# Performance work log

Hardware: AMD Instinct MI355X
Metric: run time of the kernel (lower is better)

Reference implementation:

```python
import jax, jax.numpy as jnp
import numpy as np

IN_FEATURES = 4096
OUT_FEATURES = 4096
BLOCK_SIZE = 16
E2M1_VALUES = jnp.array([0.0, 0.5, 1.0, 1.5, 2.0, 3.0, 4.0, 6.0], dtype=jnp.float32)


def dequantize_nvfp4(weight_packed, weight_scales, out_features, in_features, block_size, dtype):
    # Unpack two 4-bit codes per byte: even positions = high nibble, odd = low nibble
    p = weight_packed.astype(jnp.int32)
    high = (p >> 4) & 15
    low = p & 15
    unpacked = jnp.stack([high, low], axis=-1).reshape(-1)  # [out*in]
    sign = ((unpacked >> 3) & 1).astype(dtype)
    mag_code = unpacked & 7
    magnitude = E2M1_VALUES.astype(dtype)[mag_code]
    vals = jnp.where(sign == 1, -magnitude, magnitude)
    # Expand per-block E4M3 scales (repeat_interleave)
    scales_expanded = jnp.repeat(weight_scales.astype(dtype), block_size)
    w = vals * scales_expanded
    return w.reshape(out_features, in_features)


def setup_inputs() -> dict:
    key = jax.random.key(0)
    k1, k2, k3, k4 = jax.random.split(key, 4)
    x = jax.random.normal(k1, (4, 2048, IN_FEATURES), dtype=jnp.float32)
    weight_packed = jax.random.randint(k2, (OUT_FEATURES * IN_FEATURES // 2,), 0, 256, dtype=jnp.int32)
    weight_scales = jax.random.uniform(k3, (OUT_FEATURES * IN_FEATURES // BLOCK_SIZE,), dtype=jnp.float32)
    bias = jax.random.normal(k4, (OUT_FEATURES,), dtype=jnp.float32)
    return {"x": x, "weight_packed": weight_packed, "weight_scales": weight_scales, "bias": bias}


def reference(x, weight_packed, weight_scales, bias):
    w = dequantize_nvfp4(weight_packed, weight_scales, OUT_FEATURES, IN_FEATURES, BLOCK_SIZE, x.dtype)
    # F.linear: y = x @ w.T + bias
    return jnp.einsum('bsi,oi->bso', x, w) + bias
```

## Files before the change

kernel.cpp:

```cpp
#include <hip/hip_runtime.h>
#include <cstdint>
#include <cstddef>

#define MDIM 8192
#define NDIM 4096
#define KDIM 4096

typedef __attribute__((ext_vector_type(8))) __bf16 bf16x8;
typedef __attribute__((ext_vector_type(4))) float floatx4;

typedef __attribute__((address_space(3))) void lds_t;
typedef __attribute__((address_space(1))) void glb_t;

__device__ __forceinline__ unsigned short f32_to_bf16(float f) {
  unsigned int u = __float_as_uint(f);
  u += 0x7FFFu + ((u >> 16) & 1u);
  return (unsigned short)(u >> 16);
}

__device__ __forceinline__ float fp4_mag(int c) {
  int e = (c >> 1) & 3, m = c & 1;
  int sh = e ? (e - 1) : 0;
  return e ? 0.5f * (float)((2 + m) << sh) : 0.5f * (float)m;
}

__global__ __launch_bounds__(256) void conv_x_kernel(const float* __restrict__ x,
                                                     unsigned short* __restrict__ xb) {
  const int t = blockIdx.x * 256 + threadIdx.x;
  const float4* src = (const float4*)x + (size_t)t * 2;
  float4 a = src[0], b = src[1];
  union { unsigned short us[8]; uint4 u4; } o;
  o.us[0] = f32_to_bf16(a.x); o.us[1] = f32_to_bf16(a.y);
  o.us[2] = f32_to_bf16(a.z); o.us[3] = f32_to_bf16(a.w);
  o.us[4] = f32_to_bf16(b.x); o.us[5] = f32_to_bf16(b.y);
  o.us[6] = f32_to_bf16(b.z); o.us[7] = f32_to_bf16(b.w);
  ((uint4*)xb)[t] = o.u4;
}

__global__ __launch_bounds__(256) void dequant_kernel(const int* __restrict__ packed,
                                                      const float* __restrict__ scales,
                                                      unsigned short* __restrict__ wb) {
  const int t = blockIdx.x * 256 + threadIdx.x;
  const int4* p = (const int4*)packed + (size_t)t * 2;
  int4 pa = p[0], pb = p[1];
  float s = scales[t];
  int bytes[8] = {pa.x, pa.y, pa.z, pa.w, pb.x, pb.y, pb.z, pb.w};
  union { unsigned short us[16]; uint4 u4[2]; } o;
#pragma unroll
  for (int i = 0; i < 8; ++i) {
    int by = bytes[i] & 255;
    int hi = by >> 4, lo = by & 15;
    float vh = fp4_mag(hi & 7) * s; if (hi & 8) vh = -vh;
    float vl = fp4_mag(lo & 7) * s; if (lo & 8) vl = -vl;
    o.us[2 * i]     = f32_to_bf16(vh);
    o.us[2 * i + 1] = f32_to_bf16(vl);
  }
  uint4* dst = (uint4*)(wb + (size_t)t * 16);
  dst[0] = o.u4[0]; dst[1] = o.u4[1];
}

__global__ __launch_bounds__(512) void gemm256_kernel(const __bf16* __restrict__ A,
                                                      const __bf16* __restrict__ B,
                                                      const float* __restrict__ bias,
                                                      float* __restrict__ C) {
  __shared__ __bf16 ldsbuf[65536];
  __bf16* As = ldsbuf;
  __bf16* Bs = ldsbuf + 32768;

  const int t = threadIdx.x;
  const int wave = t >> 6, lane = t & 63;
  const int quad = lane >> 4, r16 = lane & 15;
  const int wr = wave >> 2, wc = wave & 3;

  const int bid = blockIdx.x;
  const int wg = (bid & 7) * 64 + (bid >> 3);
  const int m0 = (wg >> 4) * 256, n0 = (wg & 15) * 256;

  const int swzS = ((t >> 3) & 7) << 4;
  const int b0 = (t * 16) ^ swzS;
  const int b1 = (8192 + t * 16) ^ swzS;
  const int row0 = b0 >> 6, col0 = (b0 & 63) >> 1;
  const int row1 = b1 >> 6, col1 = (b1 & 63) >> 1;

  const __bf16* pa0 = A + (size_t)(m0 + row0) * KDIM + col0;
  const __bf16* pa1 = A + (size_t)(m0 + row1) * KDIM + col1;
  const __bf16* pb0 = B + (size_t)(n0 + row0) * KDIM + col0;
  const __bf16* pb1 = B + (size_t)(n0 + row1) * KDIM + col1;

  const int swzR = ((r16 >> 1) & 7) << 4;
  const int offAe = ((((wr * 128 + r16) * 64) + quad * 16) ^ swzR) >> 1;
  const int offBe = ((((wc * 64  + r16) * 64) + quad * 16) ^ swzR) >> 1;

  floatx4 acc[8][4] = {};

#define STAGE(TT) do {                                                                              \
    const int _kk = (TT) * 32;                                                                      \
    __bf16* _ab = As + ((TT) & 3) * 8192;                                                           \
    __bf16* _bb = Bs + ((TT) & 3) * 8192;                                                           \
    __builtin_amdgcn_global_load_lds((const glb_t*)(pa0 + _kk), (lds_t*)(_ab + wave * 512), 16, 0, 0);        \
    __builtin_amdgcn_global_load_lds((const glb_t*)(pa1 + _kk), (lds_t*)(_ab + 4096 + wave * 512), 16, 0, 0); \
    __builtin_amdgcn_global_load_lds((const glb_t*)(pb0 + _kk), (lds_t*)(_bb + wave * 512), 16, 0, 0);        \
    __builtin_amdgcn_global_load_lds((const glb_t*)(pb1 + _kk), (lds_t*)(_bb + 4096 + wave * 512), 16, 0, 0); \
  } while (0)

#define BARRIER() asm volatile("s_barrier" ::: "memory")

#define COMPUTE(TT) do {                                                          \
    const __bf16* _a = As + ((TT) & 3) * 8192;                                    \
    const __bf16* _b = Bs + ((TT) & 3) * 8192;                                    \
    bf16x8 af[8], bfv[4];                                                         \
    _Pragma("unroll")                                                             \
    for (int i = 0; i < 8; ++i) af[i] = *(const bf16x8*)(_a + offAe + i * 512);   \
    _Pragma("unroll")                                                             \
    for (int j = 0; j < 4; ++j) bfv[j] = *(const bf16x8*)(_b + offBe + j * 512);  \
    __builtin_amdgcn_s_setprio(1);                                                \
    _Pragma("unroll")                                                             \
    for (int i = 0; i < 8; ++i) {                                                 \
      _Pragma("unroll")                                                           \
      for (int j = 0; j < 4; ++j)                                                 \
        acc[i][j] = __builtin_amdgcn_mfma_f32_16x16x32_bf16(af[i], bfv[j], acc[i][j], 0, 0, 0); \
    }                                                                             \
    __builtin_amdgcn_s_setprio(0);                                                \
    BARRIER();                                                                    \
  } while (0)

  STAGE(0); STAGE(1); STAGE(2);

  for (int T = 0; T < 125; ++T) {
    STAGE(T + 3);
    asm volatile("s_waitcnt vmcnt(12)" ::: "memory");
    BARRIER();
    COMPUTE(T);
  }
  asm volatile("s_waitcnt vmcnt(8)" ::: "memory");
  BARRIER();
  COMPUTE(125);
  asm volatile("s_waitcnt vmcnt(4)" ::: "memory");
  BARRIER();
  COMPUTE(126);
  asm volatile("s_waitcnt vmcnt(0)" ::: "memory");
  BARRIER();
  COMPUTE(127);

#undef STAGE
#undef BARRIER
#undef COMPUTE

  float bv[4];
#pragma unroll
  for (int j = 0; j < 4; ++j) bv[j] = bias[n0 + wc * 64 + j * 16 + r16];
#pragma unroll
  for (int i = 0; i < 8; ++i) {
    const int gm = m0 + wr * 128 + i * 16 + quad * 4;
#pragma unroll
    for (int j = 0; j < 4; ++j) {
      float* cp = C + (size_t)gm * NDIM + (n0 + wc * 64 + j * 16 + r16);
#pragma unroll
      for (int r = 0; r < 4; ++r)
        cp[(size_t)r * NDIM] = acc[i][j][r] + bv[j];
    }
  }
}

__global__ __launch_bounds__(256) void fused_fallback(const float* __restrict__ x,
                                                      const int* __restrict__ packed,
                                                      const float* __restrict__ scales,
                                                      const float* __restrict__ bias,
                                                      float* __restrict__ out) {
  const int n = blockIdx.x * 256 + threadIdx.x;
  const int m = blockIdx.y;
  const float* xr = x + (size_t)m * KDIM;
  const int* pr = packed + (size_t)n * (KDIM / 2);
  const float* sc = scales + (size_t)n * (KDIM / 16);
  float acc = 0.f;
  for (int kb = 0; kb < KDIM / 16; ++kb) {
    float s = sc[kb];
    float part = 0.f;
#pragma unroll
    for (int i = 0; i < 8; ++i) {
      int by = pr[kb * 8 + i] & 255;
      int hi = by >> 4, lo = by & 15;
      float vh = fp4_mag(hi & 7); if (hi & 8) vh = -vh;
      float vl = fp4_mag(lo & 7); if (lo & 8) vl = -vl;
      part += xr[kb * 16 + 2 * i] * vh + xr[kb * 16 + 2 * i + 1] * vl;
    }
    acc += s * part;
  }
  out[(size_t)m * NDIM + n] = acc + bias[n];
}

extern "C" void kernel_launch(void* const* d_in, const int* in_sizes, int n_in,
                              void* d_out, int out_size, void* d_ws, size_t ws_size,
                              hipStream_t stream) {
  const float* x      = (const float*)d_in[0];
  const int*   packed = (const int*)d_in[1];
  const float* scales = (const float*)d_in[2];
  const float* bias   = (const float*)d_in[3];
  float* out = (float*)d_out;

  const size_t needA = (size_t)MDIM * KDIM * 2;
  const size_t needW = (size_t)NDIM * KDIM * 2;

  if (ws_size >= needA + needW) {
    unsigned short* xb = (unsigned short*)d_ws;
    unsigned short* wb = (unsigned short*)((char*)d_ws + needA);
    conv_x_kernel<<<(MDIM * KDIM / 8) / 256, 256, 0, stream>>>(x, xb);
    dequant_kernel<<<(NDIM * KDIM / 16) / 256, 256, 0, stream>>>(packed, scales, wb);
    dim3 grid((MDIM / 256) * (NDIM / 256));
    gemm256_kernel<<<grid, 512, 0, stream>>>((const __bf16*)xb, (const __bf16*)wb, bias, out);
  } else {
    dim3 grid(NDIM / 256, MDIM);
    fused_fallback<<<grid, 256, 0, stream>>>(x, packed, scales, bias, out);
  }
}
```

Baseline: 502.7 us.

## Split GEMM K-tile into two half phases with interleaved async loads

Restructures the main loop so each K-tile is processed in two halves of 4 A-fragments each, interleaving the global-to-LDS loads for A and B of a future stage between the halves, with extra barriers and explicit lgkmcnt waits. This cuts live A-fragment registers and, together with launch_bounds(512,2), aims for higher occupancy and finer-grained overlap of memory traffic with MFMA work. The cost is double the barriers per tile. The 64K bf16 LDS buffer (128 KiB) may also prevent a second workgroup per CU from fitting, which would leave the occupancy hint with little or no benefit.

Result: no change. 493.2 us (-1.9%).

```diff
diff --git a/kernel.cpp b/kernel.cpp
--- a/kernel.cpp
+++ b/kernel.cpp
@@ -59,10 +59,10 @@
   dst[0] = o.u4[0]; dst[1] = o.u4[1];
 }
 
-__global__ __launch_bounds__(512) void gemm256_kernel(const __bf16* __restrict__ A,
-                                                      const __bf16* __restrict__ B,
-                                                      const float* __restrict__ bias,
-                                                      float* __restrict__ C) {
+__global__ __launch_bounds__(512, 2) void gemm256_kernel(const __bf16* __restrict__ A,
+                                                         const __bf16* __restrict__ B,
+                                                         const float* __restrict__ bias,
+                                                         float* __restrict__ C) {
   __shared__ __bf16 ldsbuf[65536];
   __bf16* As = ldsbuf;
   __bf16* Bs = ldsbuf + 32768;
@@ -93,58 +93,81 @@
 
   floatx4 acc[8][4] = {};
 
-#define STAGE(TT) do {                                                                              \
-    const int _kk = (TT) * 32;                                                                      \
-    __bf16* _ab = As + ((TT) & 3) * 8192;                                                           \
-    __bf16* _bb = Bs + ((TT) & 3) * 8192;                                                           \
-    __builtin_amdgcn_global_load_lds((const glb_t*)(pa0 + _kk), (lds_t*)(_ab + wave * 512), 16, 0, 0);        \
-    __builtin_amdgcn_global_load_lds((const glb_t*)(pa1 + _kk), (lds_t*)(_ab + 4096 + wave * 512), 16, 0, 0); \
-    __builtin_amdgcn_global_load_lds((const glb_t*)(pb0 + _kk), (lds_t*)(_bb + wave * 512), 16, 0, 0);        \
-    __builtin_amdgcn_global_load_lds((const glb_t*)(pb1 + _kk), (lds_t*)(_bb + 4096 + wave * 512), 16, 0, 0); \
-  } while (0)
-
-#define BARRIER() asm volatile("s_barrier" ::: "memory")
-
-#define COMPUTE(TT) do {                                                          \
+#pragma unroll
+  for (int p = 0; p < 3; ++p) {
+    __bf16* _ab = As + p * 8192;
+    __bf16* _bb = Bs + p * 8192;
+    __builtin_amdgcn_global_load_lds((const glb_t*)(pa0 + p * 32), (lds_t*)(_ab + wave * 512), 16, 0, 0);
+    __builtin_amdgcn_global_load_lds((const glb_t*)(pa1 + p * 32), (lds_t*)(_ab + 4096 + wave * 512), 16, 0, 0);
+    __builtin_amdgcn_global_load_lds((const glb_t*)(pb0 + p * 32), (lds_t*)(_bb + wave * 512), 16, 0, 0);
+    __builtin_amdgcn_global_load_lds((const glb_t*)(pb1 + p * 32), (lds_t*)(_bb + 4096 + wave * 512), 16, 0, 0);
+  }
+  asm volatile("s_waitcnt vmcnt(8)" ::: "memory");
+  __builtin_amdgcn_s_barrier();
+
+  const __bf16* sa0 = pa0 + 96;
+  const __bf16* sa1 = pa1 + 96;
+  const __bf16* sb0 = pb0 + 96;
+  const __bf16* sb1 = pb1 + 96;
+
+#define TILE(TT, DO_STAGE, VMASM) do {                                            \
     const __bf16* _a = As + ((TT) & 3) * 8192;                                    \
     const __bf16* _b = Bs + ((TT) & 3) * 8192;                                    \
-    bf16x8 af[8], bfv[4];                                                         \
-    _Pragma("unroll")                                                             \
-    for (int i = 0; i < 8; ++i) af[i] = *(const bf16x8*)(_a + offAe + i * 512);   \
+    __bf16* _sa = As + (((TT) + 3) & 3) * 8192;                                   \
+    __bf16* _sb = Bs + (((TT) + 3) & 3) * 8192;                                   \
+    bf16x8 af[4], bfv[4];                                                         \
+                                               \
+    _Pragma("unroll")                                                             \
+    for (int i = 0; i < 4; ++i) af[i] = *(const bf16x8*)(_a + offAe + i * 512);   \
     _Pragma("unroll")                                                             \
     for (int j = 0; j < 4; ++j) bfv[j] = *(const bf16x8*)(_b + offBe + j * 512);  \
+    if (DO_STAGE) {                                                               \
+      __builtin_amdgcn_global_load_lds((const glb_t*)sa0, (lds_t*)(_sa + wave * 512), 16, 0, 0);        \
+      __builtin_amdgcn_global_load_lds((const glb_t*)sa1, (lds_t*)(_sa + 4096 + wave * 512), 16, 0, 0); \
+    }                                                                             \
+    __builtin_amdgcn_s_barrier();                                                 \
+    asm volatile("s_waitcnt lgkmcnt(0)" ::: "memory");                            \
+    __builtin_amdgcn_sched_barrier(0);                                            \
     __builtin_amdgcn_s_setprio(1);                                                \
     _Pragma("unroll")                                                             \
-    for (int i = 0; i < 8; ++i) {                                                 \
+    for (int i = 0; i < 4; ++i) {                                                 \
       _Pragma("unroll")                                                           \
       for (int j = 0; j < 4; ++j)                                                 \
         acc[i][j] = __builtin_amdgcn_mfma_f32_16x16x32_bf16(af[i], bfv[j], acc[i][j], 0, 0, 0); \
     }                                                                             \
     __builtin_amdgcn_s_setprio(0);                                                \
-    BARRIER();                                                                    \
+    __builtin_amdgcn_s_barrier();                                                 \
+                                               \
+    _Pragma("unroll")                                                             \
+    for (int i = 0; i < 4; ++i) af[i] = *(const bf16x8*)(_a + offAe + (4 + i) * 512); \
+    if (DO_STAGE) {                                                               \
+      __builtin_amdgcn_global_load_lds((const glb_t*)sb0, (lds_t*)(_sb + wave * 512), 16, 0, 0);        \
+      __builtin_amdgcn_global_load_lds((const glb_t*)sb1, (lds_t*)(_sb + 4096 + wave * 512), 16, 0, 0); \
+    }                                                                             \
+    __builtin_amdgcn_s_barrier();                                                 \
+    asm volatile("s_waitcnt lgkmcnt(0)" ::: "memory");                            \
+    __builtin_amdgcn_sched_barrier(0);                                            \
+    __builtin_amdgcn_s_setprio(1);                                                \
+    _Pragma("unroll")                                                             \
+    for (int i = 0; i < 4; ++i) {                                                 \
+      _Pragma("unroll")                                                           \
+      for (int j = 0; j < 4; ++j)                                                 \
+        acc[4 + i][j] = __builtin_amdgcn_mfma_f32_16x16x32_bf16(af[i], bfv[j], acc[4 + i][j], 0, 0, 0); \
+    }                                                                             \
+    __builtin_amdgcn_s_setprio(0);                                                \
+    VMASM;                                                                        \
+    __builtin_amdgcn_s_barrier();                                                 \
   } while (0)
 
-  STAGE(0); STAGE(1); STAGE(2);
-
   for (int T = 0; T < 125; ++T) {
-    STAGE(T + 3);
-    asm volatile("s_waitcnt vmcnt(12)" ::: "memory");
-    BARRIER();
-    COMPUTE(T);
-  }
-  asm volatile("s_waitcnt vmcnt(8)" ::: "memory");
-  BARRIER();
-  COMPUTE(125);
-  asm volatile("s_waitcnt vmcnt(4)" ::: "memory");
-  BARRIER();
-  COMPUTE(126);
-  asm volatile("s_waitcnt vmcnt(0)" ::: "memory");
-  BARRIER();
-  COMPUTE(127);
-
-#undef STAGE
-#undef BARRIER
-#undef COMPUTE
+    TILE(T, true, asm volatile("s_waitcnt vmcnt(8)" ::: "memory"));
+    sa0 += 32; sa1 += 32; sb0 += 32; sb1 += 32;
+  }
+  TILE(125, false, asm volatile("s_waitcnt vmcnt(4)" ::: "memory"));
+  TILE(126, false, asm volatile("s_waitcnt vmcnt(0)" ::: "memory"));
+  TILE(127, false, (void)0);
+
+#undef TILE
 
   float bv[4];
 #pragma unroll
```
